# Kernel optimization log

Hardware: AMD Instinct MI355X
Metric: run time of the kernel (lower is better)

## Reference

```python
import jax, jax.numpy as jnp
import numpy as np

N_NODES = 100000
N_EDGES = 1600000
N_GRAPHS = 256


def gcn_conv(x, src, dst, edge_weight, W, b, num_nodes):
    """PyG GCNConv: add self-loops, symmetric degree normalization,
    linear transform, scatter-add aggregation, bias."""
    loop = jnp.arange(num_nodes)
    s = jnp.concatenate([src, loop])
    d = jnp.concatenate([dst, loop])
    ew = jnp.concatenate([edge_weight, jnp.ones((num_nodes,), dtype=edge_weight.dtype)])
    deg = jax.ops.segment_sum(ew, d, num_segments=num_nodes)  # [N]
    dinv = jnp.where(deg > 0, deg ** -0.5, 0.0)
    norm = dinv[s] * ew * dinv[d]  # [E+N]
    h = x @ W  # [N, out]
    msg = h[s] * norm[:, None]  # gather + scale
    out = jax.ops.segment_sum(msg, d, num_segments=num_nodes)  # scatter-add
    return out + b


def global_mean_pool(x, batch, num_graphs):
    s = jax.ops.segment_sum(x, batch, num_segments=num_graphs)
    cnt = jax.ops.segment_sum(jnp.ones((x.shape[0],), dtype=x.dtype), batch, num_segments=num_graphs)
    return s / jnp.maximum(cnt, 1.0)[:, None]


def setup_inputs() -> dict:
    key = jax.random.key(0)
    ks = jax.random.split(key, 12)
    x = jax.random.normal(ks[0], (N_NODES, 128), dtype=jnp.float32)
    edge_index = jax.random.randint(ks[1], (2, N_EDGES), 0, N_NODES, dtype=jnp.int64)
    edge_attr = jax.random.uniform(ks[2], (N_EDGES,), dtype=jnp.float32)
    batch = jnp.sort(jax.random.randint(ks[3], (N_NODES,), 0, N_GRAPHS, dtype=jnp.int64))
    def lin(k, fan_in, fan_out):
        lim = 1.0 / np.sqrt(fan_in)
        kw, kb = jax.random.split(k)
        W = jax.random.uniform(kw, (fan_in, fan_out), minval=-lim, maxval=lim, dtype=jnp.float32)
        b = jax.random.uniform(kb, (fan_out,), minval=-lim, maxval=lim, dtype=jnp.float32)
        return W, b
    W1, b1 = lin(ks[4], 128, 64)
    W2, b2 = lin(ks[5], 64, 64)
    W3, b3 = lin(ks[6], 64, 64)
    Wl, bl = lin(ks[7], 64, 10)
    return {"x": x, "edge_index": edge_index, "edge_attr": edge_attr, "batch": batch,
            "W1": W1, "b1": b1, "W2": W2, "b2": b2, "W3": W3, "b3": b3, "Wl": Wl, "bl": bl}


def reference(x, edge_index, edge_attr, batch, W1, b1, W2, b2, W3, b3, Wl, bl):
    src, dst = edge_index[0], edge_index[1]
    n = x.shape[0]
    h = jax.nn.relu(gcn_conv(x, src, dst, edge_attr, W1, b1, n))
    h = jax.nn.relu(gcn_conv(h, src, dst, edge_attr, W2, b2, n))
    h = jax.nn.relu(gcn_conv(h, src, dst, edge_attr, W3, b3, n))
    g = global_mean_pool(h, batch, N_GRAPHS)  # [G, 64]
    return g @ Wl + bl  # [G, num_classes]
```

## Files before the change

### kernel.cpp

```cpp
#include <hip/hip_runtime.h>
#include <hip/hip_bf16.h>

#define N_NODES  100000
#define N_EDGES  1600000
#define N_GRAPHS 256
#define F 64
#define NBUCK  782
#define CHUNK  4096
#define NCHUNK 391
#define GB     391


__global__ __launch_bounds__(1024) void k_hist(const int* __restrict__ dst, int* __restrict__ hist) {
    __shared__ int lh[NBUCK];
    int tid = threadIdx.x, chunk = blockIdx.x;
    for (int j = tid; j < NBUCK; j += 1024) lh[j] = 0;
    __syncthreads();
    int e0 = chunk * CHUNK;
#pragma unroll
    for (int i = 0; i < CHUNK / 1024; i++) {
        int e = e0 + i * 1024 + tid;
        if (e < N_EDGES) atomicAdd(&lh[dst[e] >> 7], 1);
    }
    __syncthreads();
    for (int j = tid; j < NBUCK; j += 1024) hist[chunk * NBUCK + j] = lh[j];
}

__global__ __launch_bounds__(512) void k_colscan(int* __restrict__ hist, int* __restrict__ btot) {
    __shared__ int ts[512];
    int b = blockIdx.x, tid = threadIdx.x;
    int v = (tid < NCHUNK) ? hist[tid * NBUCK + b] : 0;
    ts[tid] = v;
    __syncthreads();
    int x = v;
    for (int off = 1; off < 512; off <<= 1) {
        int t = (tid >= off) ? ts[tid - off] : 0;
        __syncthreads();
        x += t; ts[tid] = x;
        __syncthreads();
    }
    if (tid < NCHUNK) hist[tid * NBUCK + b] = x - v;
    if (tid == 511) btot[b] = x;
}

__global__ __launch_bounds__(512) void k_bscan_gstart(const int* __restrict__ btot, int* __restrict__ base,
                                                      const int* __restrict__ batch, int* __restrict__ gstart) {
    if (blockIdx.x == 1) {
        int g = threadIdx.x;
        if (g > N_GRAPHS) return;
        int lo = 0, hi = N_NODES;
        while (lo < hi) {
            int mid = (lo + hi) >> 1;
            if (batch[mid] < g) lo = mid + 1; else hi = mid;
        }
        gstart[g] = lo;
        return;
    }
    __shared__ int ts[256];
    int tid = threadIdx.x;
    int v[4], loc[4], run = 0;
    if (tid < 256) {
#pragma unroll
        for (int k = 0; k < 4; k++) {
            int c = tid * 4 + k;
            v[k] = (c < NBUCK) ? btot[c] : 0;
            loc[k] = run; run += v[k];
        }
        ts[tid] = run;
    }
    __syncthreads();
    int x = run;
    for (int off = 1; off < 256; off <<= 1) {
        int t = (tid >= off && tid < 256) ? ts[tid - off] : 0;
        __syncthreads();
        if (tid < 256) { x += t; ts[tid] = x; }
        __syncthreads();
    }
    if (tid < 256) {
        int texcl = x - run;
#pragma unroll
        for (int k = 0; k < 4; k++) {
            int c = tid * 4 + k;
            if (c < NBUCK) base[c] = texcl + loc[k];
        }
        if (tid == 255) base[NBUCK] = x;
    }
}

__global__ __launch_bounds__(1024) void k_partition(const int* __restrict__ src, const int* __restrict__ dst,
                                                    const float* __restrict__ ew,
                                                    const int* __restrict__ hist, const int* __restrict__ base,
                                                    long long* __restrict__ part) {
    __shared__ int cursor[NBUCK];
    int tid = threadIdx.x, chunk = blockIdx.x;
    for (int j = tid; j < NBUCK; j += 1024) cursor[j] = base[j] + hist[chunk * NBUCK + j];
    __syncthreads();
    int e0 = chunk * CHUNK;
#pragma unroll
    for (int i = 0; i < CHUNK / 1024; i++) {
        int e = e0 + i * 1024 + tid;
        if (e < N_EDGES) {
            int d = dst[e];
            int pos = atomicAdd(&cursor[d >> 7], 1);
            unsigned lo = (unsigned)src[e] | ((unsigned)(d & 127) << 17);
            long long rec = (long long)((unsigned long long)lo |
                            ((unsigned long long)__float_as_uint(ew[e]) << 32));
            part[pos] = rec;
        }
    }
}

__global__ __launch_bounds__(512) void k_deg(const long long* __restrict__ part,
                                             const int* __restrict__ base,
                                             float* __restrict__ dinv_g, int* __restrict__ row_off) {
    __shared__ float fdeg[128];
    __shared__ int   cnt[128];
    __shared__ int   sc[128];
    int b = blockIdx.x, tid = threadIdx.x;
    if (tid < 128) { fdeg[tid] = 1.0f; cnt[tid] = 0; }
    __syncthreads();
    int e0 = base[b], e1 = base[b + 1];
    for (int k = e0 + tid; k < e1; k += 512) {
        long long rec = part[k];
        int d7 = ((int)rec >> 17) & 127;
        atomicAdd(&fdeg[d7], __uint_as_float((unsigned)(rec >> 32)));
        atomicAdd(&cnt[d7], 1);
    }
    __syncthreads();
    int myc = 0, x = 0;
    if (tid < 128) {
        int node = b * 128 + tid;
        if (node < N_NODES) dinv_g[node] = rsqrtf(fdeg[tid]);
        myc = cnt[tid]; x = myc; sc[tid] = x;
    }
    __syncthreads();
    for (int off = 1; off < 128; off <<= 1) {
        int t = (tid < 128 && tid >= off) ? sc[tid - off] : 0;
        __syncthreads();
        if (tid < 128) { x += t; sc[tid] = x; }
        __syncthreads();
    }
    if (tid < 128) {
        int node = b * 128 + tid;
        if (node < N_NODES) row_off[node] = e0 + (x - myc);
    }
    if (b == 0 && tid == 0) row_off[N_NODES] = N_EDGES;
}

__global__ __launch_bounds__(512) void k_scat(const long long* __restrict__ part,
                                              const int* __restrict__ base,
                                              const float* __restrict__ dinv_g,
                                              const int* __restrict__ row_off,
                                              int2* __restrict__ esec) {
    __shared__ int cursor[128];
    int b = blockIdx.x, tid = threadIdx.x;
    if (tid < 128) {
        int node = b * 128 + tid;
        cursor[tid] = row_off[node < N_NODES ? node : N_NODES];
    }
    __syncthreads();
    int e0 = base[b], e1 = base[b + 1];
    for (int k = e0 + tid; k < e1; k += 512) {
        long long rec = part[k];
        int lo = (int)rec;
        int d7 = (lo >> 17) & 127;
        int s  = lo & 0x1FFFF;
        float w = __uint_as_float((unsigned)(rec >> 32));
        float coef = w * dinv_g[s];
        int pos = atomicAdd(&cursor[d7], 1);
        esec[pos] = make_int2(s << 7, __float_as_int(coef));
    }
    if (b == 0 && tid < 32) esec[N_EDGES + tid] = make_int2(0, 0);
}

__global__ __launch_bounds__(256) void k_gemm1(const float* __restrict__ X,
                                               const float* __restrict__ W,
                                               __hip_bfloat16* __restrict__ H) {
    constexpr int K = 128;
    constexpr int KC = 32;
    constexpr int XP = KC + 4;
    __shared__ float Xs[256 * XP];
    __shared__ float Ws[KC * F];
    const int tid  = threadIdx.x;
    const int fgrp = tid & 7;
    const int ngrp = tid >> 3;
    const int f0   = fgrp * 8;
    const int nb   = blockIdx.x * 256;

    float acc[8][8];
#pragma unroll
    for (int i = 0; i < 8; i++)
#pragma unroll
        for (int j = 0; j < 8; j++) acc[i][j] = 0.0f;

    for (int kc = 0; kc < K; kc += KC) {
        if (kc) __syncthreads();
#pragma unroll
        for (int pass = 0; pass < 8; pass++) {
            int idx = tid + pass * 256;
            int r = idx >> 3, q = idx & 7;
            int gr = nb + r; if (gr >= N_NODES) gr = N_NODES - 1;
            float4 v = *(const float4*)&X[(size_t)gr * K + kc + q * 4];
            *(float4*)&Xs[r * XP + q * 4] = v;
        }
#pragma unroll
        for (int pass = 0; pass < 2; pass++) {
            int idx = tid + pass * 256;
            float4 v = *(const float4*)&W[(size_t)(kc + (idx >> 4)) * F + (idx & 15) * 4];
            *(float4*)&Ws[idx * 4] = v;
        }
        __syncthreads();
#pragma unroll
        for (int k = 0; k < KC; k += 4) {
            float4 wa[4], wb[4];
#pragma unroll
            for (int kk = 0; kk < 4; kk++) {
                wa[kk] = *(const float4*)&Ws[(k + kk) * F + f0];
                wb[kk] = *(const float4*)&Ws[(k + kk) * F + f0 + 4];
            }
#pragma unroll
            for (int i = 0; i < 8; i++) {
                float4 xv = *(const float4*)&Xs[(ngrp + 32 * i) * XP + k];
#pragma unroll
                for (int kk = 0; kk < 4; kk++) {
                    float xk = (kk == 0) ? xv.x : (kk == 1) ? xv.y : (kk == 2) ? xv.z : xv.w;
                    acc[i][0] = fmaf(xk, wa[kk].x, acc[i][0]);
                    acc[i][1] = fmaf(xk, wa[kk].y, acc[i][1]);
                    acc[i][2] = fmaf(xk, wa[kk].z, acc[i][2]);
                    acc[i][3] = fmaf(xk, wa[kk].w, acc[i][3]);
                    acc[i][4] = fmaf(xk, wb[kk].x, acc[i][4]);
                    acc[i][5] = fmaf(xk, wb[kk].y, acc[i][5]);
                    acc[i][6] = fmaf(xk, wb[kk].z, acc[i][6]);
                    acc[i][7] = fmaf(xk, wb[kk].w, acc[i][7]);
                }
            }
        }
    }
#pragma unroll
    for (int i = 0; i < 8; i++) {
        int gn = nb + ngrp + 32 * i;
        if (gn < N_NODES) {
            __hip_bfloat16 hb[8];
#pragma unroll
            for (int j = 0; j < 8; j++) hb[j] = __float2bfloat16(acc[i][j]);
            *(uint4*)&H[(size_t)gn * F + f0] = *(uint4*)hb;
        }
    }
}

template <int K>
__global__ __launch_bounds__(256) void k_gemm(const unsigned short* __restrict__ X,
                                              const float* __restrict__ W,
                                              __hip_bfloat16* __restrict__ H) {
    constexpr int KC = 32;
    constexpr int XP = KC + 4;
    __shared__ float Xs[256 * XP];
    __shared__ float Ws[KC * F];
    const int tid  = threadIdx.x;
    const int fgrp = tid & 7;
    const int ngrp = tid >> 3;
    const int f0   = fgrp * 8;
    const int nb   = blockIdx.x * 256;

    float acc[8][8];
#pragma unroll
    for (int i = 0; i < 8; i++)
#pragma unroll
        for (int j = 0; j < 8; j++) acc[i][j] = 0.0f;

    for (int kc = 0; kc < K; kc += KC) {
        if (kc) __syncthreads();
#pragma unroll
        for (int pass = 0; pass < 4; pass++) {
            int idx = tid + pass * 256;
            int r = idx >> 2, q = idx & 3;
            int gr = nb + r; if (gr >= N_NODES) gr = N_NODES - 1;
            uint4 v = *(const uint4*)&X[(size_t)gr * K + kc + q * 8];
            float* dp = &Xs[r * XP + q * 8];
            dp[0] = __uint_as_float(v.x << 16);
            dp[1] = __uint_as_float(v.x & 0xffff0000u);
            dp[2] = __uint_as_float(v.y << 16);
            dp[3] = __uint_as_float(v.y & 0xffff0000u);
            dp[4] = __uint_as_float(v.z << 16);
            dp[5] = __uint_as_float(v.z & 0xffff0000u);
            dp[6] = __uint_as_float(v.w << 16);
            dp[7] = __uint_as_float(v.w & 0xffff0000u);
        }
#pragma unroll
        for (int pass = 0; pass < 2; pass++) {
            int idx = tid + pass * 256;
            float4 v = *(const float4*)&W[(size_t)(kc + (idx >> 4)) * F + (idx & 15) * 4];
            *(float4*)&Ws[idx * 4] = v;
        }
        __syncthreads();
#pragma unroll
        for (int k = 0; k < KC; k += 4) {
            float4 wa[4], wb[4];
#pragma unroll
            for (int kk = 0; kk < 4; kk++) {
                wa[kk] = *(const float4*)&Ws[(k + kk) * F + f0];
                wb[kk] = *(const float4*)&Ws[(k + kk) * F + f0 + 4];
            }
#pragma unroll
            for (int i = 0; i < 8; i++) {
                float4 xv = *(const float4*)&Xs[(ngrp + 32 * i) * XP + k];
#pragma unroll
                for (int kk = 0; kk < 4; kk++) {
                    float xk = (kk == 0) ? xv.x : (kk == 1) ? xv.y : (kk == 2) ? xv.z : xv.w;
                    acc[i][0] = fmaf(xk, wa[kk].x, acc[i][0]);
                    acc[i][1] = fmaf(xk, wa[kk].y, acc[i][1]);
                    acc[i][2] = fmaf(xk, wa[kk].z, acc[i][2]);
                    acc[i][3] = fmaf(xk, wa[kk].w, acc[i][3]);
                    acc[i][4] = fmaf(xk, wb[kk].x, acc[i][4]);
                    acc[i][5] = fmaf(xk, wb[kk].y, acc[i][5]);
                    acc[i][6] = fmaf(xk, wb[kk].z, acc[i][6]);
                    acc[i][7] = fmaf(xk, wb[kk].w, acc[i][7]);
                }
            }
        }
    }
#pragma unroll
    for (int i = 0; i < 8; i++) {
        int gn = nb + ngrp + 32 * i;
        if (gn < N_NODES) {
            __hip_bfloat16 hb[8];
#pragma unroll
            for (int j = 0; j < 8; j++) hb[j] = __float2bfloat16(acc[i][j]);
            *(uint4*)&H[(size_t)gn * F + f0] = *(uint4*)hb;
        }
    }
}

#define ACC8(A, C, H)                                            \
    A[0] = fmaf(C, __uint_as_float((H).x << 16),         A[0]);  \
    A[1] = fmaf(C, __uint_as_float((H).x & 0xffff0000u), A[1]);  \
    A[2] = fmaf(C, __uint_as_float((H).y << 16),         A[2]);  \
    A[3] = fmaf(C, __uint_as_float((H).y & 0xffff0000u), A[3]);  \
    A[4] = fmaf(C, __uint_as_float((H).z << 16),         A[4]);  \
    A[5] = fmaf(C, __uint_as_float((H).z & 0xffff0000u), A[5]);  \
    A[6] = fmaf(C, __uint_as_float((H).w << 16),         A[6]);  \
    A[7] = fmaf(C, __uint_as_float((H).w & 0xffff0000u), A[7]);

__global__ __launch_bounds__(256) void k_agg(const __hip_bfloat16* __restrict__ H,
                                             const int* __restrict__ row_off,
                                             const int2* __restrict__ esec,
                                             const float* __restrict__ dinv,
                                             const float* __restrict__ bias,
                                             __hip_bfloat16* __restrict__ O) {
    int wv   = threadIdx.x >> 6;
    int lane = threadIdx.x & 63;
    int node = blockIdx.x * 4 + wv;
    int q  = lane >> 3;
    int f8 = lane & 7;
    int r0 = __builtin_amdgcn_readfirstlane(row_off[node]);
    int r1 = __builtin_amdgcn_readfirstlane(row_off[node + 1]);
    const char* Hbase = (const char*)H;
    const int fb = f8 << 4;

    float a[8];
#pragma unroll
    for (int u = 0; u < 8; u++) a[u] = 0.0f;

    int iters = (r1 - r0 + 7) >> 3;
    int j = r0 + q;

    int2 ev = esec[j < N_EDGES ? j : N_EDGES];

    for (int it = 0; it < iters; it++) {
        int nj = j + 8;
        int2 en = esec[nj < N_EDGES ? nj : N_EDGES];
        bool t = j < r1;
        float c    = t ? __int_as_float(ev.y) : 0.0f;
        unsigned o = t ? (unsigned)ev.x : 0u;
        uint4 h = *(const uint4*)(Hbase + o + fb);
        ACC8(a, c, h)
        ev = en; j = nj;
    }
#pragma unroll
    for (int m = 8; m < 64; m <<= 1) {
#pragma unroll
        for (int u = 0; u < 8; u++) a[u] += __shfl_xor(a[u], m);
    }
    if (q == 0) {
        float di = dinv[node];
        float di2 = di * di;
        uint4 hs = *(const uint4*)(Hbase + (size_t)node * 128 + fb);
        float hv[8];
        hv[0] = __uint_as_float(hs.x << 16);
        hv[1] = __uint_as_float(hs.x & 0xffff0000u);
        hv[2] = __uint_as_float(hs.y << 16);
        hv[3] = __uint_as_float(hs.y & 0xffff0000u);
        hv[4] = __uint_as_float(hs.z << 16);
        hv[5] = __uint_as_float(hs.z & 0xffff0000u);
        hv[6] = __uint_as_float(hs.w << 16);
        hv[7] = __uint_as_float(hs.w & 0xffff0000u);
        const float4* bp = (const float4*)(bias + f8 * 8);
        float4 bv0 = bp[0], bv1 = bp[1];
        float r[8];
        r[0] = fmaxf(fmaf(a[0], di, fmaf(di2, hv[0], bv0.x)), 0.0f);
        r[1] = fmaxf(fmaf(a[1], di, fmaf(di2, hv[1], bv0.y)), 0.0f);
        r[2] = fmaxf(fmaf(a[2], di, fmaf(di2, hv[2], bv0.z)), 0.0f);
        r[3] = fmaxf(fmaf(a[3], di, fmaf(di2, hv[3], bv0.w)), 0.0f);
        r[4] = fmaxf(fmaf(a[4], di, fmaf(di2, hv[4], bv1.x)), 0.0f);
        r[5] = fmaxf(fmaf(a[5], di, fmaf(di2, hv[5], bv1.y)), 0.0f);
        r[6] = fmaxf(fmaf(a[6], di, fmaf(di2, hv[6], bv1.z)), 0.0f);
        r[7] = fmaxf(fmaf(a[7], di, fmaf(di2, hv[7], bv1.w)), 0.0f);
        __hip_bfloat16 hb[8];
#pragma unroll
        for (int u = 0; u < 8; u++) hb[u] = __float2bfloat16(r[u]);
        *(uint4*)&O[(size_t)node * F + f8 * 8] = *(uint4*)hb;
    }
}

__global__ __launch_bounds__(512) void k_pool_linear(const __hip_bfloat16* __restrict__ H,
                                                     const int* __restrict__ gstart,
                                                     const float* __restrict__ Wl,
                                                     const float* __restrict__ bl,
                                                     float* __restrict__ out) {
    int g = blockIdx.x;
    int beg = gstart[g], end = gstart[g + 1];
    int lane = threadIdx.x & 63, wv = threadIdx.x >> 6;
    float acc = 0.0f;
    for (int r = beg + wv; r < end; r += 8)
        acc += __bfloat162float(H[(size_t)r * F + lane]);
    __shared__ float s[8][F];
    s[wv][lane] = acc;
    __syncthreads();
    if (wv == 0) {
        float tot = 0.0f;
#pragma unroll
        for (int w = 0; w < 8; w++) tot += s[w][lane];
        float cntf = (float)(end - beg);
        float p = tot / fmaxf(cntf, 1.0f);
        for (int c = 0; c < 10; c++) {
            float v = p * Wl[lane * 10 + c];
            for (int off = 32; off; off >>= 1) v += __shfl_down(v, off);
            if (lane == 0) out[g * 10 + c] = v + bl[c];
        }
    }
}


extern "C" void kernel_launch(void* const* d_in, const int* in_sizes, int n_in,
                              void* d_out, int out_size, void* d_ws, size_t ws_size,
                              hipStream_t stream) {
    const float* x    = (const float*)d_in[0];
    const int*   ei   = (const int*)d_in[1];
    const float* ea   = (const float*)d_in[2];
    const int*   bat  = (const int*)d_in[3];
    const float* W1   = (const float*)d_in[4];
    const float* b1   = (const float*)d_in[5];
    const float* W2   = (const float*)d_in[6];
    const float* b2   = (const float*)d_in[7];
    const float* W3   = (const float*)d_in[8];
    const float* b3   = (const float*)d_in[9];
    const float* Wl   = (const float*)d_in[10];
    const float* bl   = (const float*)d_in[11];
    float* out = (float*)d_out;

    const int* src = ei;
    const int* dst = ei + N_EDGES;

    char* ws = (char*)d_ws;
    size_t off = 0;
    auto carve = [&](size_t bytes) {
        void* p = ws + off;
        off += (bytes + 255) & ~(size_t)255;
        return p;
    };
    float*          dinv    = (float*)carve(N_NODES * 4);
    int*            row_off = (int*)  carve((N_NODES + 1) * 4);
    int2*           esec    = (int2*) carve(((size_t)N_EDGES + 32) * 8);
    __hip_bfloat16* hbuf    = (__hip_bfloat16*)carve((size_t)N_NODES * F * 2);
    __hip_bfloat16* obuf    = (__hip_bfloat16*)carve((size_t)N_NODES * F * 2);
    long long*      part    = (long long*)carve((size_t)N_EDGES * 8);
    int*            hist    = (int*)  carve((size_t)NCHUNK * NBUCK * 4);
    int*            btot    = (int*)  carve((NBUCK + 8) * 4);
    int*            base    = (int*)  carve((NBUCK + 8) * 4);
    int*            gstart  = (int*)  carve((N_GRAPHS + 1) * 4);
    (void)ws_size; (void)in_sizes; (void)n_in; (void)out_size;

    k_hist        <<<NCHUNK, 1024, 0, stream>>>(dst, hist);
    k_colscan     <<<NBUCK,  512,  0, stream>>>(hist, btot);
    k_bscan_gstart<<<2,      512,  0, stream>>>(btot, base, bat, gstart);
    k_partition   <<<NCHUNK, 1024, 0, stream>>>(src, dst, ea, hist, base, part);
    k_deg         <<<NBUCK,  512,  0, stream>>>(part, base, dinv, row_off);
    k_scat        <<<NBUCK,  512,  0, stream>>>(part, base, dinv, row_off, esec);

    k_gemm1<<<GB, 256, 0, stream>>>(x, W1, hbuf);
    k_agg<<<N_NODES / 4, 256, 0, stream>>>(hbuf, row_off, esec, dinv, b1, obuf);
    k_gemm<64><<<GB, 256, 0, stream>>>((const unsigned short*)obuf, W2, hbuf);
    k_agg<<<N_NODES / 4, 256, 0, stream>>>(hbuf, row_off, esec, dinv, b2, obuf);
    k_gemm<64><<<GB, 256, 0, stream>>>((const unsigned short*)obuf, W3, hbuf);
    k_agg<<<N_NODES / 4, 256, 0, stream>>>(hbuf, row_off, esec, dinv, b3, obuf);

    k_pool_linear<<<N_GRAPHS, 512, 0, stream>>>(obuf, gstart, Wl, bl, out);
}
```

Baseline: 399.7 us.

## Sort nodes by degree and process 8 nodes per wavefront in aggregation

Fuses the degree and edge-scatter kernels into one, and moves the dinv[src] edge scaling into the GEMM epilogue so H is stored pre-scaled by dinv. Adds a counting sort of nodes by in-degree, producing a permutation. The aggregation kernel now gives each 8-lane group its own node, with nodes of similar degree sharing a wavefront, and unrolls the edge loop by four. The aim is to remove the wasted lanes and cross-lane reductions of one-node-per-wave aggregation, at the cost of three extra small sort kernels and less coalesced output writes.

```diff
diff --git a/kernel.cpp b/kernel.cpp
--- a/kernel.cpp
+++ b/kernel.cpp
@@ -9,6 +9,8 @@
 #define CHUNK  4096
 #define NCHUNK 391
 #define GB     391
+#define NBIN   64
+#define NCHN   98
 
 
 __global__ __launch_bounds__(1024) void k_hist(const int* __restrict__ dst, int* __restrict__ hist) {
@@ -110,12 +112,14 @@
     }
 }
 
-__global__ __launch_bounds__(512) void k_deg(const long long* __restrict__ part,
-                                             const int* __restrict__ base,
-                                             float* __restrict__ dinv_g, int* __restrict__ row_off) {
+__global__ __launch_bounds__(512) void k_degscat(const long long* __restrict__ part,
+                                                 const int* __restrict__ base,
+                                                 float* __restrict__ dinv_g, int* __restrict__ row_off,
+                                                 int2* __restrict__ esec) {
     __shared__ float fdeg[128];
     __shared__ int   cnt[128];
     __shared__ int   sc[128];
+    __shared__ int   cursor[128];
     int b = blockIdx.x, tid = threadIdx.x;
     if (tid < 128) { fdeg[tid] = 1.0f; cnt[tid] = 0; }
     __syncthreads();
@@ -142,39 +146,77 @@
     }
     if (tid < 128) {
         int node = b * 128 + tid;
-        if (node < N_NODES) row_off[node] = e0 + (x - myc);
+        int ro = e0 + (x - myc);
+        if (node < N_NODES) row_off[node] = ro;
+        cursor[tid] = ro;
     }
     if (b == 0 && tid == 0) row_off[N_NODES] = N_EDGES;
-}
-
-__global__ __launch_bounds__(512) void k_scat(const long long* __restrict__ part,
-                                              const int* __restrict__ base,
-                                              const float* __restrict__ dinv_g,
-                                              const int* __restrict__ row_off,
-                                              int2* __restrict__ esec) {
-    __shared__ int cursor[128];
-    int b = blockIdx.x, tid = threadIdx.x;
-    if (tid < 128) {
-        int node = b * 128 + tid;
-        cursor[tid] = row_off[node < N_NODES ? node : N_NODES];
-    }
-    __syncthreads();
-    int e0 = base[b], e1 = base[b + 1];
+    __syncthreads();
     for (int k = e0 + tid; k < e1; k += 512) {
         long long rec = part[k];
         int lo = (int)rec;
         int d7 = (lo >> 17) & 127;
         int s  = lo & 0x1FFFF;
-        float w = __uint_as_float((unsigned)(rec >> 32));
-        float coef = w * dinv_g[s];
         int pos = atomicAdd(&cursor[d7], 1);
-        esec[pos] = make_int2(s << 7, __float_as_int(coef));
+        esec[pos] = make_int2(s << 7, (int)(unsigned)(rec >> 32));
     }
     if (b == 0 && tid < 32) esec[N_EDGES + tid] = make_int2(0, 0);
+}
+
+
+__global__ __launch_bounds__(1024) void k_nhist(const int* __restrict__ row_off, int* __restrict__ nhist) {
+    __shared__ int lh[NBIN];
+    int tid = threadIdx.x, c = blockIdx.x;
+    if (tid < NBIN) lh[tid] = 0;
+    __syncthreads();
+    int n = c * 1024 + tid;
+    if (n < N_NODES) {
+        int len = row_off[n + 1] - row_off[n];
+        int bin = len; if (bin > NBIN - 1) bin = NBIN - 1;
+        atomicAdd(&lh[bin], 1);
+    }
+    __syncthreads();
+    if (tid < NBIN) nhist[c * NBIN + tid] = lh[tid];
+}
+
+__global__ __launch_bounds__(1024) void k_nscan(int* __restrict__ nhist) {
+    __shared__ int h[NCHN * NBIN];
+    __shared__ int tot[NBIN];
+    int tid = threadIdx.x;
+    for (int i = tid; i < NCHN * NBIN; i += 1024) h[i] = nhist[i];
+    __syncthreads();
+    if (tid < NBIN) {
+        int run = 0;
+        for (int c = 0; c < NCHN; c++) { int v = h[c * NBIN + tid]; h[c * NBIN + tid] = run; run += v; }
+        tot[tid] = run;
+    }
+    __syncthreads();
+    if (tid == 0) {
+        int run = 0;
+        for (int b = 0; b < NBIN; b++) { int v = tot[b]; tot[b] = run; run += v; }
+    }
+    __syncthreads();
+    for (int i = tid; i < NCHN * NBIN; i += 1024) nhist[i] = h[i] + tot[i & (NBIN - 1)];
+}
+
+__global__ __launch_bounds__(1024) void k_nscat(const int* __restrict__ row_off, const int* __restrict__ nhist,
+                                                int* __restrict__ perm) {
+    __shared__ int cur[NBIN];
+    int tid = threadIdx.x, c = blockIdx.x;
+    if (tid < NBIN) cur[tid] = nhist[c * NBIN + tid];
+    __syncthreads();
+    int n = c * 1024 + tid;
+    if (n < N_NODES) {
+        int len = row_off[n + 1] - row_off[n];
+        int bin = len; if (bin > NBIN - 1) bin = NBIN - 1;
+        int pos = atomicAdd(&cur[bin], 1);
+        perm[pos] = n;
+    }
 }
 
 __global__ __launch_bounds__(256) void k_gemm1(const float* __restrict__ X,
                                                const float* __restrict__ W,
+                                               const float* __restrict__ dinv,
                                                __hip_bfloat16* __restrict__ H) {
     constexpr int K = 128;
     constexpr int KC = 32;
@@ -240,9 +282,10 @@
     for (int i = 0; i < 8; i++) {
         int gn = nb + ngrp + 32 * i;
         if (gn < N_NODES) {
+            float di = dinv[gn];
             __hip_bfloat16 hb[8];
 #pragma unroll
-            for (int j = 0; j < 8; j++) hb[j] = __float2bfloat16(acc[i][j]);
+            for (int j = 0; j < 8; j++) hb[j] = __float2bfloat16(acc[i][j] * di);
             *(uint4*)&H[(size_t)gn * F + f0] = *(uint4*)hb;
         }
     }
@@ -251,6 +294,7 @@
 template <int K>
 __global__ __launch_bounds__(256) void k_gemm(const unsigned short* __restrict__ X,
                                               const float* __restrict__ W,
+                                              const float* __restrict__ dinv,
                                               __hip_bfloat16* __restrict__ H) {
     constexpr int KC = 32;
     constexpr int XP = KC + 4;
@@ -323,9 +367,10 @@
     for (int i = 0; i < 8; i++) {
         int gn = nb + ngrp + 32 * i;
         if (gn < N_NODES) {
+            float di = dinv[gn];
             __hip_bfloat16 hb[8];
 #pragma unroll
-            for (int j = 0; j < 8; j++) hb[j] = __float2bfloat16(acc[i][j]);
+            for (int j = 0; j < 8; j++) hb[j] = __float2bfloat16(acc[i][j] * di);
             *(uint4*)&H[(size_t)gn * F + f0] = *(uint4*)hb;
         }
     }
@@ -341,75 +386,80 @@
     A[6] = fmaf(C, __uint_as_float((H).w << 16),         A[6]);  \
     A[7] = fmaf(C, __uint_as_float((H).w & 0xffff0000u), A[7]);
 
-__global__ __launch_bounds__(256) void k_agg(const __hip_bfloat16* __restrict__ H,
+__global__ __launch_bounds__(256) void k_agg(const __hip_bfloat16* __restrict__ Hd,
                                              const int* __restrict__ row_off,
                                              const int2* __restrict__ esec,
                                              const float* __restrict__ dinv,
                                              const float* __restrict__ bias,
+                                             const int* __restrict__ perm,
                                              __hip_bfloat16* __restrict__ O) {
+    int lane = threadIdx.x & 63;
     int wv   = threadIdx.x >> 6;
-    int lane = threadIdx.x & 63;
-    int node = blockIdx.x * 4 + wv;
-    int q  = lane >> 3;
-    int f8 = lane & 7;
-    int r0 = __builtin_amdgcn_readfirstlane(row_off[node]);
-    int r1 = __builtin_amdgcn_readfirstlane(row_off[node + 1]);
-    const char* Hbase = (const char*)H;
+    int ns   = lane >> 3;
+    int f8   = lane & 7;
+    int np   = blockIdx.x * 32 + wv * 8 + ns;
+    int node = perm[np];
+    int r0 = row_off[node];
+    int r1 = row_off[node + 1];
+    int ml = r1 - r0;
+    ml = max(ml, __shfl_xor(ml, 8));
+    ml = max(ml, __shfl_xor(ml, 16));
+    ml = max(ml, __shfl_xor(ml, 32));
+    const char* Hb = (const char*)Hd;
     const int fb = f8 << 4;
 
     float a[8];
 #pragma unroll
     for (int u = 0; u < 8; u++) a[u] = 0.0f;
 
-    int iters = (r1 - r0 + 7) >> 3;
-    int j = r0 + q;
-
-    int2 ev = esec[j < N_EDGES ? j : N_EDGES];
-
-    for (int it = 0; it < iters; it++) {
-        int nj = j + 8;
-        int2 en = esec[nj < N_EDGES ? nj : N_EDGES];
-        bool t = j < r1;
-        float c    = t ? __int_as_float(ev.y) : 0.0f;
-        unsigned o = t ? (unsigned)ev.x : 0u;
-        uint4 h = *(const uint4*)(Hbase + o + fb);
-        ACC8(a, c, h)
-        ev = en; j = nj;
-    }
-#pragma unroll
-    for (int m = 8; m < 64; m <<= 1) {
-#pragma unroll
-        for (int u = 0; u < 8; u++) a[u] += __shfl_xor(a[u], m);
-    }
-    if (q == 0) {
-        float di = dinv[node];
-        float di2 = di * di;
-        uint4 hs = *(const uint4*)(Hbase + (size_t)node * 128 + fb);
-        float hv[8];
-        hv[0] = __uint_as_float(hs.x << 16);
-        hv[1] = __uint_as_float(hs.x & 0xffff0000u);
-        hv[2] = __uint_as_float(hs.y << 16);
-        hv[3] = __uint_as_float(hs.y & 0xffff0000u);
-        hv[4] = __uint_as_float(hs.z << 16);
-        hv[5] = __uint_as_float(hs.z & 0xffff0000u);
-        hv[6] = __uint_as_float(hs.w << 16);
-        hv[7] = __uint_as_float(hs.w & 0xffff0000u);
-        const float4* bp = (const float4*)(bias + f8 * 8);
-        float4 bv0 = bp[0], bv1 = bp[1];
-        float r[8];
-        r[0] = fmaxf(fmaf(a[0], di, fmaf(di2, hv[0], bv0.x)), 0.0f);
-        r[1] = fmaxf(fmaf(a[1], di, fmaf(di2, hv[1], bv0.y)), 0.0f);
-        r[2] = fmaxf(fmaf(a[2], di, fmaf(di2, hv[2], bv0.z)), 0.0f);
-        r[3] = fmaxf(fmaf(a[3], di, fmaf(di2, hv[3], bv0.w)), 0.0f);
-        r[4] = fmaxf(fmaf(a[4], di, fmaf(di2, hv[4], bv1.x)), 0.0f);
-        r[5] = fmaxf(fmaf(a[5], di, fmaf(di2, hv[5], bv1.y)), 0.0f);
-        r[6] = fmaxf(fmaf(a[6], di, fmaf(di2, hv[6], bv1.z)), 0.0f);
-        r[7] = fmaxf(fmaf(a[7], di, fmaf(di2, hv[7], bv1.w)), 0.0f);
-        __hip_bfloat16 hb[8];
-#pragma unroll
-        for (int u = 0; u < 8; u++) hb[u] = __float2bfloat16(r[u]);
-        *(uint4*)&O[(size_t)node * F + f8 * 8] = *(uint4*)hb;
-    }
+    int nw = (ml + 3) >> 2;
+    int j = r0;
+    for (int w = 0; w < nw; w++) {
+        int2 e0 = esec[j     < r1 ? j     : N_EDGES];
+        int2 e1 = esec[j + 1 < r1 ? j + 1 : N_EDGES];
+        int2 e2 = esec[j + 2 < r1 ? j + 2 : N_EDGES];
+        int2 e3 = esec[j + 3 < r1 ? j + 3 : N_EDGES];
+        uint4 h0 = *(const uint4*)(Hb + (unsigned)e0.x + fb);
+        uint4 h1 = *(const uint4*)(Hb + (unsigned)e1.x + fb);
+        uint4 h2 = *(const uint4*)(Hb + (unsigned)e2.x + fb);
+        uint4 h3 = *(const uint4*)(Hb + (unsigned)e3.x + fb);
+        float c0 = __int_as_float(e0.y);
+        float c1 = __int_as_float(e1.y);
+        float c2 = __int_as_float(e2.y);
+        float c3 = __int_as_float(e3.y);
+        ACC8(a, c0, h0)
+        ACC8(a, c1, h1)
+        ACC8(a, c2, h2)
+        ACC8(a, c3, h3)
+        j += 4;
+    }
+
+    float di = dinv[node];
+    uint4 hs = *(const uint4*)(Hb + (size_t)node * 128 + fb);
+    float hv[8];
+    hv[0] = __uint_as_float(hs.x << 16);
+    hv[1] = __uint_as_float(hs.x & 0xffff0000u);
+    hv[2] = __uint_as_float(hs.y << 16);
+    hv[3] = __uint_as_float(hs.y & 0xffff0000u);
+    hv[4] = __uint_as_float(hs.z << 16);
+    hv[5] = __uint_as_float(hs.z & 0xffff0000u);
+    hv[6] = __uint_as_float(hs.w << 16);
+    hv[7] = __uint_as_float(hs.w & 0xffff0000u);
+    const float4* bp = (const float4*)(bias + f8 * 8);
+    float4 bv0 = bp[0], bv1 = bp[1];
+    float r[8];
+    r[0] = fmaxf(fmaf(di, a[0] + hv[0], bv0.x), 0.0f);
+    r[1] = fmaxf(fmaf(di, a[1] + hv[1], bv0.y), 0.0f);
+    r[2] = fmaxf(fmaf(di, a[2] + hv[2], bv0.z), 0.0f);
+    r[3] = fmaxf(fmaf(di, a[3] + hv[3], bv0.w), 0.0f);
+    r[4] = fmaxf(fmaf(di, a[4] + hv[4], bv1.x), 0.0f);
+    r[5] = fmaxf(fmaf(di, a[5] + hv[5], bv1.y), 0.0f);
+    r[6] = fmaxf(fmaf(di, a[6] + hv[6], bv1.z), 0.0f);
+    r[7] = fmaxf(fmaf(di, a[7] + hv[7], bv1.w), 0.0f);
+    __hip_bfloat16 hb[8];
+#pragma unroll
+    for (int u = 0; u < 8; u++) hb[u] = __float2bfloat16(r[u]);
+    *(uint4*)&O[(size_t)node * F + f8 * 8] = *(uint4*)hb;
 }
 
 __global__ __launch_bounds__(512) void k_pool_linear(const __hip_bfloat16* __restrict__ H,
@@ -478,21 +528,25 @@
     int*            btot    = (int*)  carve((NBUCK + 8) * 4);
     int*            base    = (int*)  carve((NBUCK + 8) * 4);
     int*            gstart  = (int*)  carve((N_GRAPHS + 1) * 4);
+    int*            nhist   = (int*)  carve((size_t)NCHN * NBIN * 4);
+    int*            perm    = (int*)  carve((size_t)N_NODES * 4);
     (void)ws_size; (void)in_sizes; (void)n_in; (void)out_size;
 
     k_hist        <<<NCHUNK, 1024, 0, stream>>>(dst, hist);
     k_colscan     <<<NBUCK,  512,  0, stream>>>(hist, btot);
     k_bscan_gstart<<<2,      512,  0, stream>>>(btot, base, bat, gstart);
     k_partition   <<<NCHUNK, 1024, 0, stream>>>(src, dst, ea, hist, base, part);
-    k_deg         <<<NBUCK,  512,  0, stream>>>(part, base, dinv, row_off);
-    k_scat        <<<NBUCK,  512,  0, stream>>>(part, base, dinv, row_off, esec);
-
-    k_gemm1<<<GB, 256, 0, stream>>>(x, W1, hbuf);
-    k_agg<<<N_NODES / 4, 256, 0, stream>>>(hbuf, row_off, esec, dinv, b1, obuf);
-    k_gemm<64><<<GB, 256, 0, stream>>>((const unsigned short*)obuf, W2, hbuf);
-    k_agg<<<N_NODES / 4, 256, 0, stream>>>(hbuf, row_off, esec, dinv, b2, obuf);
-    k_gemm<64><<<GB, 256, 0, stream>>>((const unsigned short*)obuf, W3, hbuf);
-    k_agg<<<N_NODES / 4, 256, 0, stream>>>(hbuf, row_off, esec, dinv, b3, obuf);
+    k_degscat     <<<NBUCK,  512,  0, stream>>>(part, base, dinv, row_off, esec);
+    k_nhist       <<<NCHN,   1024, 0, stream>>>(row_off, nhist);
+    k_nscan       <<<1,      1024, 0, stream>>>(nhist);
+    k_nscat       <<<NCHN,   1024, 0, stream>>>(row_off, nhist, perm);
+
+    k_gemm1<<<GB, 256, 0, stream>>>(x, W1, dinv, hbuf);
+    k_agg<<<N_NODES / 32, 256, 0, stream>>>(hbuf, row_off, esec, dinv, b1, perm, obuf);
+    k_gemm<64><<<GB, 256, 0, stream>>>((const unsigned short*)obuf, W2, dinv, hbuf);
+    k_agg<<<N_NODES / 32, 256, 0, stream>>>(hbuf, row_off, esec, dinv, b2, perm, obuf);
+    k_gemm<64><<<GB, 256, 0, stream>>>((const unsigned short*)obuf, W3, dinv, hbuf);
+    k_agg<<<N_NODES / 32, 256, 0, stream>>>(hbuf, row_off, esec, dinv, b3, perm, obuf);
 
     k_pool_linear<<<N_GRAPHS, 512, 0, stream>>>(obuf, gstart, Wl, bl, out);
 }
```

Result: faster. 375.4 us (-6.1%).
